# Kernel tuning notes

Hardware: AMD Instinct MI355X
Metric: run time of the kernel (lower is better)

## Reference

```python
import jax, jax.numpy as jnp
import numpy as np


def setup_inputs() -> dict:
    key = jax.random.key(0)
    k1, k2, k3, k4 = jax.random.split(key, 4)
    B, T, C, H = 16, 2048, 1024, 128
    x = jax.random.normal(k1, (B, T, C), dtype=jnp.float32)
    # bias-free Dense kernels (stored as [in, out] like keras)
    s = 1.0 / np.sqrt(C)
    Wk = jax.random.normal(k2, (C, H), dtype=jnp.float32) * s
    Wq = jax.random.normal(k3, (C, H), dtype=jnp.float32) * s
    Wv = jax.random.normal(k4, (C, H), dtype=jnp.float32) * s
    return {"x": x, "Wk": Wk, "Wq": Wq, "Wv": Wv}


def reference(x, Wk, Wq, Wv):
    # single-head causal self-attention (dropout inactive at inference)
    B, T, C = x.shape
    H = Wk.shape[-1]
    k = jnp.einsum('btc,ch->bth', x, Wk)   # [B,T,H]
    q = jnp.einsum('btc,ch->bth', x, Wq)
    v = jnp.einsum('btc,ch->bth', x, Wv)
    scale = 1.0 / jnp.sqrt(jnp.float32(H))
    wei = jnp.einsum('bqh,bkh->bqk', q, k) * scale          # [B,T,T]
    causal = jnp.tril(jnp.ones((T, T), dtype=bool))
    wei = jnp.where(causal, wei, -jnp.inf)
    wei = jax.nn.softmax(wei, axis=-1)
    out = jnp.einsum('bqk,bkh->bqh', wei, v)                # [B,T,H]
    return out
```

## Files before the change

kernel.cpp:

```cpp
#include <hip/hip_runtime.h>
#include <hip/hip_bf16.h>

typedef __bf16 bf16x8_t __attribute__((ext_vector_type(8)));
typedef __bf16 bf16x4_t __attribute__((ext_vector_type(4)));
typedef float  f32x4_t  __attribute__((ext_vector_type(4)));

#define MFMA_16x16x32_BF16(A, B, C) __builtin_amdgcn_mfma_f32_16x16x32_bf16((A), (B), (C), 0, 0, 0)

static constexpr int B_ = 16;
static constexpr int T_ = 2048;
static constexpr int C_ = 1024;
static constexpr int H_ = 128;
static constexpr long M_ = (long)B_ * T_;

__device__ __forceinline__ void gload_lds16(const void* g, void* l)
{
    __builtin_amdgcn_global_load_lds(
        (const __attribute__((address_space(1))) void*)g,
        (__attribute__((address_space(3))) void*)l, 16, 0, 0);
}

__global__ __launch_bounds__(128) void wt_kernel(
    const float* __restrict__ Wq, const float* __restrict__ Wk,
    const float* __restrict__ Wv, __bf16* __restrict__ WT)
{
    const int z = blockIdx.y;
    const float* __restrict__ W = (z == 0) ? Wq : (z == 1) ? Wk : Wv;
    const int h  = threadIdx.x;
    const int c0 = blockIdx.x * 8;
    bf16x8_t v;
    #pragma unroll
    for (int j = 0; j < 8; ++j)
        v[j] = (__bf16)W[(c0 + j) * H_ + h];
    *(bf16x8_t*)&WT[((long)z * H_ + h) * C_ + c0] = v;
}

__global__ __launch_bounds__(256, 4) void proj_kernel(
    const float*  __restrict__ x,
    const __bf16* __restrict__ WT,
    __bf16* __restrict__ qo,
    __bf16* __restrict__ ko,
    __bf16* __restrict__ vo)
{
    __shared__ float  XS[2][64 * 32];
    __shared__ __bf16 WS[2][192 * 32];

    const int tid  = threadIdx.x;
    const int w    = tid >> 6;
    const int lane = tid & 63;
    const int m16  = lane & 15;
    const int quad = lane >> 4;
    const int wr   = w >> 1;
    const int wc   = w & 1;

    const int  rb = blockIdx.x >> 1;
    const int  cb = blockIdx.x & 1;
    const long r0 = (long)rb * 64;
    const int  n0 = cb * 192;

    const int xl_row = lane >> 3;
    const int xl_u   = (lane & 7) ^ xl_row;
    const int wl_row = lane >> 2;
    const int wl_u   = (lane & 3) ^ ((lane >> 3) & 3);

    f32x4_t acc[2][6];
    #pragma unroll
    for (int hh = 0; hh < 2; ++hh)
        #pragma unroll
        for (int j = 0; j < 6; ++j) acc[hh][j] = f32x4_t{0, 0, 0, 0};

#define ISSUE(T, BUF)                                                        \
    {                                                                        \
        const int k0_ = (T) * 32;                                            \
        _Pragma("unroll")                                                    \
        for (int ch = 0; ch < 2; ++ch) {                                     \
            const int rbx = w * 16 + ch * 8;                                 \
            gload_lds16(&x[(r0 + rbx + xl_row) * C_ + k0_ + xl_u * 4],       \
                        &XS[BUF][rbx * 32]);                                 \
        }                                                                    \
        _Pragma("unroll")                                                    \
        for (int ch = 0; ch < 3; ++ch) {                                     \
            const int rbw = w * 48 + ch * 16;                                \
            gload_lds16(&WT[(long)(n0 + rbw + wl_row) * C_ + k0_ + wl_u * 8],\
                        &WS[BUF][rbw * 32]);                                 \
        }                                                                    \
    }

    ISSUE(0, 0);
    __syncthreads();

    const int asw = m16 & 7;
    const int qsw = (quad ^ ((m16 >> 1) & 3)) << 3;

    for (int t = 0; t < 32; ++t) {
        const int cur = t & 1;
        if (t < 31) ISSUE(t + 1, cur ^ 1);

        bf16x8_t a[2];
        #pragma unroll
        for (int hh = 0; hh < 2; ++hh) {
            const int row = wr * 32 + hh * 16 + m16;
            f32x4_t lo = *(const f32x4_t*)&XS[cur][row * 32 + (((quad * 2 + 0) ^ asw) << 2)];
            f32x4_t hi = *(const f32x4_t*)&XS[cur][row * 32 + (((quad * 2 + 1) ^ asw) << 2)];
            #pragma unroll
            for (int jj = 0; jj < 4; ++jj) {
                a[hh][jj]     = (__bf16)lo[jj];
                a[hh][4 + jj] = (__bf16)hi[jj];
            }
        }
        #pragma unroll
        for (int j = 0; j < 6; ++j) {
            const int row = wc * 96 + j * 16 + m16;
            bf16x8_t b = *(const bf16x8_t*)&WS[cur][row * 32 + qsw];
            #pragma unroll
            for (int hh = 0; hh < 2; ++hh)
                acc[hh][j] = MFMA_16x16x32_BF16(a[hh], b, acc[hh][j]);
        }

        __syncthreads();
    }
#undef ISSUE

    #pragma unroll
    for (int hh = 0; hh < 2; ++hh) {
        const long rbase = r0 + wr * 32 + hh * 16 + quad * 4;
        #pragma unroll
        for (int j = 0; j < 6; ++j) {
            const int nt = cb * 12 + wc * 6 + j;
            const int z  = nt >> 3;
            const int h  = (nt & 7) * 16 + m16;
            if (z < 2) {
                __bf16* __restrict__ o = z ? ko : qo;
                #pragma unroll
                for (int r = 0; r < 4; ++r)
                    o[(rbase + r) * H_ + h] = (__bf16)acc[hh][j][r];
            } else {
                long bb = rbase >> 11, tt = rbase & 2047;
                bf16x4_t pk;
                #pragma unroll
                for (int r = 0; r < 4; ++r) pk[r] = (__bf16)acc[hh][j][r];
                *(bf16x4_t*)&vo[bb * (H_ * (long)T_) + h * (long)T_ + tt] = pk;
            }
        }
    }
}

__global__ __launch_bounds__(256) void attn_kernel(
    const __bf16* __restrict__ q,
    const __bf16* __restrict__ k,
    const __bf16* __restrict__ vT,
    float* __restrict__ out)
{
    __shared__ __bf16 KS[64 * 136];
    __shared__ __bf16 VS[128 * 72];
    __shared__ __bf16 PS[4][16 * 72];

    const int L   = blockIdx.x;
    const int b   = L & 15;
    const int Lh  = L >> 4;
    const int qb  = (Lh < 16) ? (31 - Lh) : (Lh - 16);

    const int tid  = threadIdx.x;
    const int w    = tid >> 6;
    const int lane = tid & 63;
    const int m16  = lane & 15;
    const int quad = lane >> 4;
    const int koff = quad * 8;

    const __bf16* __restrict__ qp = q  + (long)b * T_ * H_;
    const __bf16* __restrict__ kp = k  + (long)b * T_ * H_;
    const __bf16* __restrict__ vp = vT + (long)b * H_ * T_;

    const int q0w = qb * 64 + w * 16;
    const int qg  = q0w + m16;

    bf16x8_t qfr[4];
    #pragma unroll
    for (int s = 0; s < 4; ++s)
        qfr[s] = *(const bf16x8_t*)&qp[(q0w + m16) * H_ + s * 32 + koff];

    f32x4_t acc[8];
    #pragma unroll
    for (int i = 0; i < 8; ++i) acc[i] = f32x4_t{0, 0, 0, 0};
    float mrun = -1e30f, lrun = 0.f;

    __bf16* Pb = &PS[w][0];
    const float SC = 0.08838834764831845f;
    const int kend = qb * 64 + 64;

    const int krow = tid >> 4, kc16 = tid & 15;
    const int vrow = tid >> 3, vc8  = tid & 7;

    for (int tk0 = 0; tk0 < kend; tk0 += 64) {
        __syncthreads();
        #pragma unroll
        for (int ch = 0; ch < 4; ++ch) {
            int r = krow + ch * 16;
            *(bf16x8_t*)&KS[r * 136 + kc16 * 8] =
                *(const bf16x8_t*)&kp[(tk0 + r) * H_ + kc16 * 8];
        }
        #pragma unroll
        for (int ch = 0; ch < 4; ++ch) {
            int hh = vrow + ch * 32;
            *(bf16x8_t*)&VS[hh * 72 + vc8 * 8] =
                *(const bf16x8_t*)&vp[hh * (long)T_ + tk0 + vc8 * 8];
        }
        __syncthreads();

        f32x4_t st[4];
        #pragma unroll
        for (int kt = 0; kt < 4; ++kt) {
            f32x4_t s = f32x4_t{0, 0, 0, 0};
            #pragma unroll
            for (int sI = 0; sI < 4; ++sI) {
                bf16x8_t kf = *(const bf16x8_t*)&KS[(kt * 16 + m16) * 136 + sI * 32 + koff];
                s = MFMA_16x16x32_BF16(kf, qfr[sI], s);
            }
            st[kt] = s;
        }

        float vv[4][4];
        if (tk0 + 63 <= q0w) {
            #pragma unroll
            for (int kt = 0; kt < 4; ++kt)
                #pragma unroll
                for (int r = 0; r < 4; ++r)
                    vv[kt][r] = st[kt][r] * SC;
        } else {
            #pragma unroll
            for (int kt = 0; kt < 4; ++kt)
                #pragma unroll
                for (int r = 0; r < 4; ++r) {
                    int kg = tk0 + kt * 16 + quad * 4 + r;
                    vv[kt][r] = (kg <= qg) ? st[kt][r] * SC : -1e30f;
                }
        }

        float mloc = -1e30f;
        #pragma unroll
        for (int kt = 0; kt < 4; ++kt)
            #pragma unroll
            for (int r = 0; r < 4; ++r)
                mloc = fmaxf(mloc, vv[kt][r]);
        mloc = fmaxf(mloc, __shfl_xor(mloc, 16, 64));
        mloc = fmaxf(mloc, __shfl_xor(mloc, 32, 64));

        float mnew = fmaxf(mrun, mloc);
        float al   = __expf(mrun - mnew);
        float psum = 0.f;
        #pragma unroll
        for (int kt = 0; kt < 4; ++kt) {
            bf16x4_t pk;
            #pragma unroll
            for (int r = 0; r < 4; ++r) {
                float p = __expf(vv[kt][r] - mnew);
                psum += p;
                pk[r] = (__bf16)p;
            }
            *(bf16x4_t*)&Pb[m16 * 72 + kt * 16 + quad * 4] = pk;
        }
        psum += __shfl_xor(psum, 16, 64);
        psum += __shfl_xor(psum, 32, 64);
        mrun = mnew;
        lrun = lrun * al + psum;

        #pragma unroll
        for (int i = 0; i < 8; ++i)
            #pragma unroll
            for (int r = 0; r < 4; ++r)
                acc[i][r] *= al;

        #pragma unroll
        for (int half = 0; half < 2; ++half) {
            bf16x8_t pa = *(const bf16x8_t*)&Pb[m16 * 72 + half * 32 + koff];
            #pragma unroll
            for (int i = 0; i < 8; ++i) {
                bf16x8_t vf = *(const bf16x8_t*)&VS[(i * 16 + m16) * 72 + half * 32 + koff];
                acc[i] = MFMA_16x16x32_BF16(vf, pa, acc[i]);
            }
        }
    }

    float* __restrict__ ob = out + (long)b * T_ * H_;
    const float inv = 1.f / lrun;
    #pragma unroll
    for (int i = 0; i < 8; ++i) {
        f32x4_t o;
        #pragma unroll
        for (int r = 0; r < 4; ++r) o[r] = acc[i][r] * inv;
        *(f32x4_t*)&ob[(q0w + m16) * H_ + i * 16 + quad * 4] = o;
    }
}

extern "C" void kernel_launch(void* const* d_in, const int* in_sizes, int n_in,
                              void* d_out, int out_size, void* d_ws, size_t ws_size,
                              hipStream_t stream)
{
    const float* x  = (const float*)d_in[0];
    const float* Wk = (const float*)d_in[1];
    const float* Wq = (const float*)d_in[2];
    const float* Wv = (const float*)d_in[3];

    __bf16* qws = (__bf16*)d_ws;
    __bf16* kws = qws + M_ * H_;
    __bf16* vws = kws + M_ * H_;
    __bf16* WT  = vws + (long)B_ * H_ * T_;
    float*  out = (float*)d_out;

    wt_kernel  <<<dim3(C_ / 8, 3), 128, 0, stream>>>(Wq, Wk, Wv, WT);
    proj_kernel<<<dim3((int)(M_ / 64) * 2), 256, 0, stream>>>(x, WT, qws, kws, vws);
    attn_kernel<<<dim3(512), 256, 0, stream>>>(qws, kws, vws, out);
}
```

Measured before the change: 300.0 us.

## Pre-swizzle weights into MFMA fragment order and load B directly from global

```diff
diff --git a/kernel.cpp b/kernel.cpp
--- a/kernel.cpp
+++ b/kernel.cpp
@@ -20,48 +20,48 @@
         (__attribute__((address_space(3))) void*)l, 16, 0, 0);
 }
 
-__global__ __launch_bounds__(128) void wt_kernel(
+__global__ __launch_bounds__(256) void wt_kernel(
     const float* __restrict__ Wq, const float* __restrict__ Wk,
-    const float* __restrict__ Wv, __bf16* __restrict__ WT)
-{
-    const int z = blockIdx.y;
+    const float* __restrict__ Wv, __bf16* __restrict__ WB)
+{
+    const int pair = blockIdx.x * 4 + (threadIdx.x >> 6);
+    const int lane = threadIdx.x & 63;
+    const int m16  = lane & 15;
+    const int quad = lane >> 4;
+    const int nt   = pair >> 5;
+    const int t    = pair & 31;
+    const int z    = nt >> 3;
+    const int h    = (nt & 7) * 16 + m16;
     const float* __restrict__ W = (z == 0) ? Wq : (z == 1) ? Wk : Wv;
-    const int h  = threadIdx.x;
-    const int c0 = blockIdx.x * 8;
+
     bf16x8_t v;
     #pragma unroll
-    for (int j = 0; j < 8; ++j)
-        v[j] = (__bf16)W[(c0 + j) * H_ + h];
-    *(bf16x8_t*)&WT[((long)z * H_ + h) * C_ + c0] = v;
+    for (int e = 0; e < 8; ++e)
+        v[e] = (__bf16)W[(t * 32 + quad * 8 + e) * H_ + h];
+    *(bf16x8_t*)&WB[((long)pair * 64 + lane) * 8] = v;
 }
 
 __global__ __launch_bounds__(256, 4) void proj_kernel(
     const float*  __restrict__ x,
-    const __bf16* __restrict__ WT,
+    const __bf16* __restrict__ WB,
     __bf16* __restrict__ qo,
     __bf16* __restrict__ ko,
     __bf16* __restrict__ vo)
 {
-    __shared__ float  XS[2][64 * 32];
-    __shared__ __bf16 WS[2][192 * 32];
+    __shared__ float XS[2][32 * 32];
 
     const int tid  = threadIdx.x;
     const int w    = tid >> 6;
     const int lane = tid & 63;
     const int m16  = lane & 15;
     const int quad = lane >> 4;
-    const int wr   = w >> 1;
-    const int wc   = w & 1;
-
-    const int  rb = blockIdx.x >> 1;
-    const int  cb = blockIdx.x & 1;
-    const long r0 = (long)rb * 64;
-    const int  n0 = cb * 192;
+
+    const long r0 = (long)blockIdx.x * 32;
 
     const int xl_row = lane >> 3;
     const int xl_u   = (lane & 7) ^ xl_row;
-    const int wl_row = lane >> 2;
-    const int wl_u   = (lane & 3) ^ ((lane >> 3) & 3);
+
+    const __bf16* __restrict__ wp = WB + ((long)(w * 6) * 32 + 0) * 512 + lane * 8;
 
     f32x4_t acc[2][6];
     #pragma unroll
@@ -69,37 +69,28 @@
         #pragma unroll
         for (int j = 0; j < 6; ++j) acc[hh][j] = f32x4_t{0, 0, 0, 0};
 
-#define ISSUE(T, BUF)                                                        \
-    {                                                                        \
-        const int k0_ = (T) * 32;                                            \
-        _Pragma("unroll")                                                    \
-        for (int ch = 0; ch < 2; ++ch) {                                     \
-            const int rbx = w * 16 + ch * 8;                                 \
-            gload_lds16(&x[(r0 + rbx + xl_row) * C_ + k0_ + xl_u * 4],       \
-                        &XS[BUF][rbx * 32]);                                 \
-        }                                                                    \
-        _Pragma("unroll")                                                    \
-        for (int ch = 0; ch < 3; ++ch) {                                     \
-            const int rbw = w * 48 + ch * 16;                                \
-            gload_lds16(&WT[(long)(n0 + rbw + wl_row) * C_ + k0_ + wl_u * 8],\
-                        &WS[BUF][rbw * 32]);                                 \
-        }                                                                    \
-    }
-
-    ISSUE(0, 0);
+#define XSTAGE(T, BUF)                                                       \
+    gload_lds16(&x[(r0 + w * 8 + xl_row) * C_ + (T) * 32 + xl_u * 4],        \
+                &XS[BUF][w * 8 * 32]);
+
+    XSTAGE(0, 0);
     __syncthreads();
 
     const int asw = m16 & 7;
-    const int qsw = (quad ^ ((m16 >> 1) & 3)) << 3;
 
     for (int t = 0; t < 32; ++t) {
         const int cur = t & 1;
-        if (t < 31) ISSUE(t + 1, cur ^ 1);
+        if (t < 31) XSTAGE(t + 1, cur ^ 1);
+
+        bf16x8_t b[6];
+        #pragma unroll
+        for (int j = 0; j < 6; ++j)
+            b[j] = *(const bf16x8_t*)(wp + ((long)j * 32 + t) * 512);
 
         bf16x8_t a[2];
         #pragma unroll
         for (int hh = 0; hh < 2; ++hh) {
-            const int row = wr * 32 + hh * 16 + m16;
+            const int row = hh * 16 + m16;
             f32x4_t lo = *(const f32x4_t*)&XS[cur][row * 32 + (((quad * 2 + 0) ^ asw) << 2)];
             f32x4_t hi = *(const f32x4_t*)&XS[cur][row * 32 + (((quad * 2 + 1) ^ asw) << 2)];
             #pragma unroll
@@ -108,25 +99,23 @@
                 a[hh][4 + jj] = (__bf16)hi[jj];
             }
         }
-        #pragma unroll
-        for (int j = 0; j < 6; ++j) {
-            const int row = wc * 96 + j * 16 + m16;
-            bf16x8_t b = *(const bf16x8_t*)&WS[cur][row * 32 + qsw];
+
+        #pragma unroll
+        for (int j = 0; j < 6; ++j)
             #pragma unroll
             for (int hh = 0; hh < 2; ++hh)
-                acc[hh][j] = MFMA_16x16x32_BF16(a[hh], b, acc[hh][j]);
-        }
+                acc[hh][j] = MFMA_16x16x32_BF16(a[hh], b[j], acc[hh][j]);
 
         __syncthreads();
     }
-#undef ISSUE
+#undef XSTAGE
 
     #pragma unroll
     for (int hh = 0; hh < 2; ++hh) {
-        const long rbase = r0 + wr * 32 + hh * 16 + quad * 4;
+        const long rbase = r0 + hh * 16 + quad * 4;
         #pragma unroll
         for (int j = 0; j < 6; ++j) {
-            const int nt = cb * 12 + wc * 6 + j;
+            const int nt = w * 6 + j;
             const int z  = nt >> 3;
             const int h  = (nt & 7) * 16 + m16;
             if (z < 2) {
@@ -304,10 +293,10 @@
     __bf16* qws = (__bf16*)d_ws;
     __bf16* kws = qws + M_ * H_;
     __bf16* vws = kws + M_ * H_;
-    __bf16* WT  = vws + (long)B_ * H_ * T_;
+    __bf16* WB  = vws + (long)B_ * H_ * T_;
     float*  out = (float*)d_out;
 
-    wt_kernel  <<<dim3(C_ / 8, 3), 128, 0, stream>>>(Wq, Wk, Wv, WT);
-    proj_kernel<<<dim3((int)(M_ / 64) * 2), 256, 0, stream>>>(x, WT, qws, kws, vws);
+    wt_kernel  <<<dim3(192), 256, 0, stream>>>(Wq, Wk, Wv, WB);
+    proj_kernel<<<dim3((int)(M_ / 32)), 256, 0, stream>>>(x, WB, qws, kws, vws);
     attn_kernel<<<dim3(512), 256, 0, stream>>>(qws, kws, vws, out);
 }
```

New measurement: 290.0 us. 3.3% less time.
